# Performance work log

Measured on AMD Instinct MI355X. Metric: run time of the kernel, lower is better.

## Reference

```python
import jax, jax.numpy as jnp
import numpy as np

N_NODES = 50000
N_HEDGES = 20000
N_EDGES = 800000
D = 128
H = 4


def setup_inputs() -> dict:
    key = jax.random.key(0)
    ks = jax.random.split(key, 12)
    s = 1.0 / np.sqrt(D)
    return {
        "x_node": jax.random.normal(ks[0], (N_NODES, D), jnp.float32),
        "x_edge": jax.random.normal(ks[1], (N_HEDGES, D), jnp.float32),
        "src": jax.random.randint(ks[2], (N_EDGES,), 0, N_NODES, jnp.int32),
        "dst": jax.random.randint(ks[3], (N_EDGES,), 0, N_HEDGES, jnp.int32),
        "Wq": jax.random.normal(ks[4], (D, D), jnp.float32) * s,
        "bq": jnp.zeros((D,), jnp.float32),
        "Wk": jax.random.normal(ks[5], (D, D), jnp.float32) * s,
        "bk": jnp.zeros((D,), jnp.float32),
        "Wv": jax.random.normal(ks[6], (D, D), jnp.float32) * s,
        "bv": jnp.zeros((D,), jnp.float32),
        "Wo": jax.random.normal(ks[7], (D, D), jnp.float32) * s,
        "bo": jnp.zeros((D,), jnp.float32),
    }


def reference(x_node, x_edge, src, dst, Wq, bq, Wk, bk, Wv, bv, Wo, bo):
    N = x_node.shape[0]
    hd = Wq.shape[1] // H  # head_dim = 32
    Q = (x_node @ Wq + bq).reshape(N, H, hd)
    K = (x_edge @ Wk + bk).reshape(-1, H, hd)
    V = (x_edge @ Wv + bv).reshape(-1, H, hd)
    # per-edge gather: [E, H, hd]
    Qe = Q[src]
    Ke = K[dst]
    Ve = V[dst]
    # per-edge, per-head scores: [E, H]
    scores = jnp.einsum("ehd,ehd->eh", Qe, Ke) / jnp.sqrt(jnp.float32(hd))
    # segment softmax grouped by src node
    m = jax.ops.segment_max(scores, src, num_segments=N)  # [N, H]
    e = jnp.exp(scores - m[src])
    z = jax.ops.segment_sum(e, src, num_segments=N)  # [N, H]
    w = e / z[src]  # [E, H]
    # weighted scatter-add of V messages back to src nodes
    msg = w[:, :, None] * Ve  # [E, H, hd]
    out = jax.ops.segment_sum(msg, src, num_segments=N)  # [N, H, hd]
    out = out.reshape(N, -1)
    return out @ Wo + bo + x_node
```

## Files before the change

kernel.cpp:

```cpp
#include <hip/hip_runtime.h>

#define D 128
#define STRIDE 6144

typedef _Float16 f16;
typedef f16 f16x2 __attribute__((ext_vector_type(2)));
typedef f16 f16x8 __attribute__((ext_vector_type(8)));
typedef float f32x4 __attribute__((ext_vector_type(4)));

__device__ inline f16x2 u2h(unsigned u) { return __builtin_bit_cast(f16x2, u); }
__device__ inline unsigned h2u(f16x2 h) { return __builtin_bit_cast(unsigned, h); }

__device__ inline float dot2(unsigned a, unsigned b, float c) {
#if __has_builtin(__builtin_amdgcn_fdot2)
    return __builtin_amdgcn_fdot2(u2h(a), u2h(b), c, false);
#else
    f16x2 x = u2h(a), y = u2h(b);
    return c + (float)x.x * (float)y.x + (float)x.y * (float)y.y;
#endif
}

__global__ void wt_prep4(const float* __restrict__ W0, const float* __restrict__ W1,
                         const float* __restrict__ W2, const float* __restrict__ W3,
                         f16* __restrict__ Wt) {
    const float* W = (blockIdx.x == 0) ? W0 : (blockIdx.x == 1) ? W1 : (blockIdx.x == 2) ? W2 : W3;
    f16* o = Wt + (size_t)blockIdx.x * D * D;
    int t = threadIdx.x;
#pragma unroll
    for (int i = 0; i < 16; ++i) {
        int f = t + i * 256;
        int k = f >> 5, c4 = f & 31;
        float4 v = *(const float4*)(W + k * D + 4 * c4);
        float vv[4] = {v.x, v.y, v.z, v.w};
#pragma unroll
        for (int e = 0; e < 4; ++e) {
            int c = 4 * c4 + e;
            o[c * D + (((k >> 3) ^ (c & 15)) << 3) + (k & 7)] = (f16)vv[e];
        }
    }
}

__device__ inline void stage_w(const f16* __restrict__ Wt, f16* Wl, int t) {
#pragma unroll
    for (int i = 0; i < 8; ++i) ((uint4*)Wl)[t + i * 256] = ((const uint4*)Wt)[t + i * 256];
}

__device__ inline void load_a_f32(const float* __restrict__ x, int gr, int nrows, int g,
                                  f16x8 a[4]) {
#pragma unroll
    for (int kc = 0; kc < 4; ++kc) {
        float4 v0 = {0.f, 0.f, 0.f, 0.f}, v1 = {0.f, 0.f, 0.f, 0.f};
        if (gr < nrows) {
            const float* xr = x + (size_t)gr * D + (kc * 4 + g) * 8;
            v0 = *(const float4*)xr;
            v1 = *(const float4*)(xr + 4);
        }
        f16x8 af;
        af[0] = (f16)v0.x; af[1] = (f16)v0.y; af[2] = (f16)v0.z; af[3] = (f16)v0.w;
        af[4] = (f16)v1.x; af[5] = (f16)v1.y; af[6] = (f16)v1.z; af[7] = (f16)v1.w;
        a[kc] = af;
    }
}

__device__ inline void mfma_ra(const f16x8 a[4], const f16* Wl, f32x4 acc[8], int lane) {
    int lr = lane & 15, g = lane >> 4;
#pragma unroll
    for (int kc = 0; kc < 4; ++kc) {
        int slot = kc * 4 + g;
#pragma unroll
        for (int ct = 0; ct < 8; ++ct) {
            int col = ct * 16 + lr;
            f16x8 bf = *(const f16x8*)(Wl + col * D + ((slot ^ (col & 15)) << 3));
            acc[ct] = __builtin_amdgcn_mfma_f32_16x16x32_f16(a[kc], bf, acc[ct], 0, 0, 0);
        }
    }
}

__global__ __launch_bounds__(256) void fused_front(
    const float* __restrict__ x_node, const float* __restrict__ x_edge,
    const int* __restrict__ src, const int* __restrict__ dst,
    const f16* __restrict__ Wt,
    const float* __restrict__ bq, const float* __restrict__ bk, const float* __restrict__ bv,
    f16* __restrict__ Qh, f16* __restrict__ KVh,
    int* __restrict__ bucket_cnt, unsigned* __restrict__ temp,
    int N, int M, int E, int nsp, int nq, float qscale) {
    __shared__ __align__(16) f16 Wl[D * D];
    int t = threadIdx.x;
    int bid = blockIdx.x;

    if (bid < nsp) {
        int* hist = (int*)Wl;
        int* lex = hist + 256;
        int* gbase = lex + 256;
        int* lcur = gbase + 256;
        int* wsum = lcur + 256;
        int* sorted = wsum + 16;
        unsigned char* sbyte = (unsigned char*)(sorted + 4096);
        hist[t] = 0;
        lcur[t] = 0;
        __syncthreads();
        int base0 = bid * 4096;
        int lim = E - base0; if (lim > 4096) lim = 4096;
        for (int i = t; i < lim; i += 256) atomicAdd(&hist[src[base0 + i] >> 8], 1);
        __syncthreads();
        int v = hist[t];
        int inc = v;
#pragma unroll
        for (int m = 1; m < 64; m <<= 1) {
            int u = __shfl_up(inc, m);
            if ((t & 63) >= m) inc += u;
        }
        if ((t & 63) == 63) wsum[t >> 6] = inc;
        __syncthreads();
        int add = 0;
#pragma unroll
        for (int w = 0; w < 4; ++w)
            if (w < (t >> 6)) add += wsum[w];
        lex[t] = add + inc - v;
        if (v) gbase[t] = atomicAdd(&bucket_cnt[t], v);
        __syncthreads();
        for (int i = t; i < lim; i += 256) {
            int s = src[base0 + i];
            int bk2 = s >> 8;
            int lp = atomicAdd(&lcur[bk2], 1);
            int sp = lex[bk2] + lp;
            sorted[sp] = ((s & 255) << 24) | dst[base0 + i];
            sbyte[sp] = (unsigned char)bk2;
        }
        __syncthreads();
        for (int i = t; i < lim; i += 256) {
            int bk2 = sbyte[i];
            int gp = gbase[bk2] + (i - lex[bk2]);
            if (gp < STRIDE) temp[(size_t)bk2 * STRIDE + gp] = (unsigned)sorted[i];
        }
    } else if (bid < nsp + nq) {
        int r0 = (bid - nsp) * 64;
        stage_w(Wt, Wl, t);
        int lane = t & 63, w = t >> 6;
        int lr = lane & 15, g = lane >> 4;
        f16x8 a[4];
        load_a_f32(x_node, r0 + 16 * w + lr, N, g, a);
        f32x4 acc[8];
#pragma unroll
        for (int i = 0; i < 8; ++i) acc[i] = (f32x4){0.f, 0.f, 0.f, 0.f};
        __syncthreads();
        mfma_ra(a, Wl, acc, lane);
        __syncthreads();
#pragma unroll
        for (int ct = 0; ct < 8; ++ct) {
            int col = ct * 16 + lr;
            float bias = bq[col];
#pragma unroll
            for (int rg = 0; rg < 4; ++rg) {
                int row = 16 * w + 4 * g + rg;
                Wl[row * D + (((col >> 3) ^ (row & 15)) << 3) + (col & 7)] =
                    (f16)((acc[ct][rg] + bias) * qscale);
            }
        }
        __syncthreads();
#pragma unroll
        for (int i = 0; i < 4; ++i) {
            int f = t + i * 256;
            int r = f >> 4, c8 = f & 15;
            if (r0 + r < N) {
                uint4 v = *(const uint4*)(Wl + r * D + ((c8 ^ (r & 15)) << 3));
                *(uint4*)(Qh + (size_t)(r0 + r) * D + 8 * c8) = v;
            }
        }
    } else {
        int r0 = (bid - nsp - nq) * 64;
        stage_w(Wt + D * D, Wl, t);
        int lane = t & 63, w = t >> 6;
        int lr = lane & 15, g = lane >> 4;
        f16x8 a[4];
        load_a_f32(x_edge, r0 + 16 * w + lr, M, g, a);
        f32x4 accK[8], accV[8];
#pragma unroll
        for (int i = 0; i < 8; ++i) accK[i] = accV[i] = (f32x4){0.f, 0.f, 0.f, 0.f};
        __syncthreads();
        mfma_ra(a, Wl, accK, lane);
        __syncthreads();
        stage_w(Wt + 2 * D * D, Wl, t);
        __syncthreads();
        mfma_ra(a, Wl, accV, lane);
        __syncthreads();
#pragma unroll
        for (int ct = 0; ct < 8; ++ct) {
            int col = ct * 16 + lr;
            float bbk = bk[col], bbv = bv[col];
            int s = col >> 2, wk = col & 3;
#pragma unroll
            for (int rg = 0; rg < 4; ++rg) {
                int row = 16 * w + 4 * g + rg;
                f16* base = Wl + row * 256 + ((s ^ (row & 15)) << 3);
                base[wk] = (f16)(accK[ct][rg] + bbk);
                base[4 + wk] = (f16)(accV[ct][rg] + bbv);
            }
        }
        __syncthreads();
#pragma unroll
        for (int i = 0; i < 8; ++i) {
            int f = t + i * 256;
            int r = f >> 5, c8 = f & 31;
            if (r0 + r < M) {
                uint4 v = *(const uint4*)(Wl + r * 256 + ((c8 ^ (r & 15)) << 3));
                *(uint4*)(KVh + (size_t)(r0 + r) * 256 + 8 * c8) = v;
            }
        }
    }
}

__global__ __launch_bounds__(256) void bucket_scatter(const unsigned* __restrict__ temp,
                                                      const int* __restrict__ bucket_cnt,
                                                      int* __restrict__ off,
                                                      int* __restrict__ csr_dst,
                                                      int N, int E, int NBUK) {
    __shared__ int nh[256], cur[256], wsum[4], sc_ex[256], dh[256], dcur[256];
    __shared__ int sorted2[STRIDE];
    __shared__ int lds_dst[STRIDE];
    int b = blockIdx.x, t = threadIdx.x;
    {
        int bc = (t < NBUK) ? bucket_cnt[t] : 0;
        int inc = bc;
#pragma unroll
        for (int m = 1; m < 64; m <<= 1) {
            int u = __shfl_up(inc, m);
            if ((t & 63) >= m) inc += u;
        }
        if ((t & 63) == 63) wsum[t >> 6] = inc;
        __syncthreads();
        int add = 0;
#pragma unroll
        for (int w = 0; w < 4; ++w)
            if (w < (t >> 6)) add += wsum[w];
        sc_ex[t] = add + inc - bc;
        nh[t] = 0;
        dh[t] = 0;
    }
    __syncthreads();
    int bo = sc_ex[b];
    int cnt = bucket_cnt[b];
    if (cnt > STRIDE) cnt = STRIDE;
    const unsigned* tb = temp + (size_t)b * STRIDE;
    for (int i = t; i < cnt; i += 256) atomicAdd(&dh[(tb[i] & 0xFFFFFFu) >> 7], 1);
    __syncthreads();
    {
        int v = dh[t];
        int inc = v;
#pragma unroll
        for (int m = 1; m < 64; m <<= 1) {
            int u = __shfl_up(inc, m);
            if ((t & 63) >= m) inc += u;
        }
        if ((t & 63) == 63) wsum[t >> 6] = inc;
        __syncthreads();
        int add = 0;
#pragma unroll
        for (int w = 0; w < 4; ++w)
            if (w < (t >> 6)) add += wsum[w];
        dcur[t] = add + inc - v;
    }
    __syncthreads();
    for (int i = t; i < cnt; i += 256) {
        unsigned it = tb[i];
        int pos = atomicAdd(&dcur[(it & 0xFFFFFFu) >> 7], 1);
        sorted2[pos] = (int)it;
    }
    __syncthreads();
    for (int i = t; i < cnt; i += 256) atomicAdd(&nh[((unsigned)sorted2[i]) >> 24], 1);
    __syncthreads();
    {
        int v = nh[t];
        int inc = v;
#pragma unroll
        for (int m = 1; m < 64; m <<= 1) {
            int u = __shfl_up(inc, m);
            if ((t & 63) >= m) inc += u;
        }
        if ((t & 63) == 63) wsum[t >> 6] = inc;
        __syncthreads();
        int add = 0;
#pragma unroll
        for (int w = 0; w < 4; ++w)
            if (w < (t >> 6)) add += wsum[w];
        int ex = add + inc - v;
        cur[t] = ex;
        int node = (b << 8) + t;
        if (node < N) off[node] = bo + ex;
        if (b == 0 && t == 0) off[N] = E;
    }
    __syncthreads();
    for (int i = t; i < cnt; i += 256) {
        unsigned it = (unsigned)sorted2[i];
        int lpos = atomicAdd(&cur[it >> 24], 1);
        lds_dst[lpos] = (int)(it & 0xFFFFFFu);
    }
    __syncthreads();
    for (int i = t; i < cnt; i += 256) csr_dst[bo + i] = lds_dst[i];
}

__global__ __launch_bounds__(256) void node_attn4(const f16* __restrict__ Qh,
                                                  const f16* __restrict__ KVh,
                                                  const int* __restrict__ off,
                                                  const int* __restrict__ csr,
                                                  f16* __restrict__ aggh, int N) {
    int wid = (int)((blockIdx.x * (size_t)blockDim.x + threadIdx.x) >> 6);
    int lane = threadIdx.x & 63;
    if (wid >= N) return;
    int j = lane & 7, g = lane >> 3;
    const f16* qp = Qh + (size_t)wid * D + 16 * j;
    uint4 qA = *(const uint4*)qp;
    uint4 qB = *(const uint4*)(qp + 8);
    int beg = off[wid], end = off[wid + 1];
    float z = 0.f;
    f16x2 a0 = {0, 0}, a1 = {0, 0}, a2 = {0, 0}, a3 = {0, 0};
    f16x2 a4 = {0, 0}, a5 = {0, 0}, a6 = {0, 0}, a7 = {0, 0};
    if (beg < end) {
        int pe = beg + g;
        int d0 = csr[(pe < end) ? pe : end - 1];
        const f16* r = KVh + (size_t)d0 * 256 + 32 * j;
        uint4 A0 = *(const uint4*)r;
        uint4 A1 = *(const uint4*)(r + 8);
        uint4 A2 = *(const uint4*)(r + 16);
        uint4 A3 = *(const uint4*)(r + 24);
        for (int p = beg; p < end; p += 8) {
            int pn = p + 8 + g;
            int dn = csr[(pn < end) ? pn : end - 1];
            const f16* rn = KVh + (size_t)dn * 256 + 32 * j;
            uint4 B0 = *(const uint4*)rn;
            uint4 B1 = *(const uint4*)(rn + 8);
            uint4 B2 = *(const uint4*)(rn + 16);
            uint4 B3 = *(const uint4*)(rn + 24);
            bool valid = (p + g) < end;
            float s = dot2(A0.x, qA.x, 0.f);
            s = dot2(A0.y, qA.y, s);
            s = dot2(A1.x, qA.z, s);
            s = dot2(A1.y, qA.w, s);
            s = dot2(A2.x, qB.x, s);
            s = dot2(A2.y, qB.y, s);
            s = dot2(A3.x, qB.z, s);
            s = dot2(A3.y, qB.w, s);
            s += __shfl_xor(s, 1);
            float eh = valid ? __expf(s) : 0.f;
            z += eh;
            f16 e16 = (f16)eh;
            f16x2 e2 = {e16, e16};
            a0 += e2 * u2h(A0.z); a1 += e2 * u2h(A0.w);
            a2 += e2 * u2h(A1.z); a3 += e2 * u2h(A1.w);
            a4 += e2 * u2h(A2.z); a5 += e2 * u2h(A2.w);
            a6 += e2 * u2h(A3.z); a7 += e2 * u2h(A3.w);
            A0 = B0; A1 = B1; A2 = B2; A3 = B3;
        }
    }
#pragma unroll
    for (int m = 8; m < 64; m <<= 1) {
        z += __shfl_xor(z, m);
        a0 += u2h(__shfl_xor((int)h2u(a0), m));
        a1 += u2h(__shfl_xor((int)h2u(a1), m));
        a2 += u2h(__shfl_xor((int)h2u(a2), m));
        a3 += u2h(__shfl_xor((int)h2u(a3), m));
        a4 += u2h(__shfl_xor((int)h2u(a4), m));
        a5 += u2h(__shfl_xor((int)h2u(a5), m));
        a6 += u2h(__shfl_xor((int)h2u(a6), m));
        a7 += u2h(__shfl_xor((int)h2u(a7), m));
    }
    if (g == 0) {
        float inv = (end > beg) ? 1.f / z : 0.f;
        uint4 o0, o1;
        o0.x = h2u((f16x2){(f16)((float)a0.x * inv), (f16)((float)a0.y * inv)});
        o0.y = h2u((f16x2){(f16)((float)a1.x * inv), (f16)((float)a1.y * inv)});
        o0.z = h2u((f16x2){(f16)((float)a2.x * inv), (f16)((float)a2.y * inv)});
        o0.w = h2u((f16x2){(f16)((float)a3.x * inv), (f16)((float)a3.y * inv)});
        o1.x = h2u((f16x2){(f16)((float)a4.x * inv), (f16)((float)a4.y * inv)});
        o1.y = h2u((f16x2){(f16)((float)a5.x * inv), (f16)((float)a5.y * inv)});
        o1.z = h2u((f16x2){(f16)((float)a6.x * inv), (f16)((float)a6.y * inv)});
        o1.w = h2u((f16x2){(f16)((float)a7.x * inv), (f16)((float)a7.y * inv)});
        f16* op = aggh + (size_t)wid * D + 16 * j;
        *(uint4*)op = o0;
        *(uint4*)(op + 8) = o1;
    }
}

__global__ __launch_bounds__(256) void gemm_o(const f16* __restrict__ aggh,
                                              const f16* __restrict__ Wt,
                                              const float* __restrict__ b,
                                              const float* __restrict__ resid,
                                              float* __restrict__ y, int nrows) {
    __shared__ __align__(16) f16 Wl[D * D];
    int t = threadIdx.x;
    int r0 = blockIdx.x * 64;
    stage_w(Wt, Wl, t);
    int lane = t & 63, w = t >> 6;
    int lr = lane & 15, g = lane >> 4;
    int gr = r0 + 16 * w + lr;
    f16x8 a[4];
#pragma unroll
    for (int kc = 0; kc < 4; ++kc) {
        uint4 v = {0u, 0u, 0u, 0u};
        if (gr < nrows) v = *(const uint4*)(aggh + (size_t)gr * D + (kc * 4 + g) * 8);
        a[kc] = __builtin_bit_cast(f16x8, v);
    }
    f32x4 acc[8];
#pragma unroll
    for (int i = 0; i < 8; ++i) acc[i] = (f32x4){0.f, 0.f, 0.f, 0.f};
    __syncthreads();
    mfma_ra(a, Wl, acc, lane);
    __syncthreads();
    float* Tf = (float*)Wl;
#pragma unroll
    for (int ct = 0; ct < 8; ++ct) {
        int col = ct * 16 + lr;
        float bias = b[col];
        int s = col >> 2, wk = col & 3;
#pragma unroll
        for (int rg = 0; rg < 4; ++rg) {
            int row = 16 * w + 4 * g + rg;
            Tf[row * D + ((s ^ (row & 15)) << 2) + wk] = acc[ct][rg] + bias;
        }
    }
    __syncthreads();
#pragma unroll
    for (int i = 0; i < 8; ++i) {
        int f = t + i * 256;
        int r = f >> 5, c4 = f & 31;
        int gr2 = r0 + r;
        if (gr2 < nrows) {
            float4 v = *(const float4*)(Tf + r * D + ((c4 ^ (r & 15)) << 2));
            float4 rv = *(const float4*)(resid + (size_t)gr2 * D + 4 * c4);
            v.x += rv.x; v.y += rv.y; v.z += rv.z; v.w += rv.w;
            *(float4*)(y + (size_t)gr2 * D + 4 * c4) = v;
        }
    }
}

extern "C" void kernel_launch(void* const* d_in, const int* in_sizes, int n_in,
                              void* d_out, int out_size, void* d_ws, size_t ws_size,
                              hipStream_t stream) {
    const float* x_node = (const float*)d_in[0];
    const float* x_edge = (const float*)d_in[1];
    const int* src = (const int*)d_in[2];
    const int* dst = (const int*)d_in[3];
    const float* Wq = (const float*)d_in[4];
    const float* bq = (const float*)d_in[5];
    const float* Wk = (const float*)d_in[6];
    const float* bk = (const float*)d_in[7];
    const float* Wv = (const float*)d_in[8];
    const float* bv = (const float*)d_in[9];
    const float* Wo = (const float*)d_in[10];
    const float* bo = (const float*)d_in[11];

    int N = in_sizes[0] / D;
    int M = in_sizes[1] / D;
    int E = in_sizes[2];
    int NBUK = (N + 255) >> 8;

    char* p = (char*)d_ws;
    auto alloc = [&](size_t bytes) -> char* {
        char* r = p;
        p += (bytes + 15) & ~(size_t)15;
        return r;
    };
    f16* Wt = (f16*)alloc((size_t)4 * D * D * 2);
    f16* Qh = (f16*)alloc((size_t)N * D * 2);
    f16* KVh = (f16*)alloc((size_t)M * 256 * 2);
    f16* aggh = (f16*)alloc((size_t)N * D * 2);
    int* bucket_cnt = (int*)alloc(256 * 4);
    int* off = (int*)alloc((size_t)(N + 1) * 4);
    unsigned* temp = (unsigned*)alloc((size_t)NBUK * STRIDE * 4);
    int* csr_dst = (int*)alloc((size_t)E * 4);
    float* out = (float*)d_out;

    hipMemsetAsync(bucket_cnt, 0, 256 * 4, stream);

    wt_prep4<<<4, 256, 0, stream>>>(Wq, Wk, Wv, Wo, Wt);

    int nq = (N + 63) / 64;
    int nkv = (M + 63) / 64;
    int nsp = (E + 4095) / 4096;
    fused_front<<<nsp + nq + nkv, 256, 0, stream>>>(x_node, x_edge, src, dst, Wt,
                                                    bq, bk, bv, Qh, KVh,
                                                    bucket_cnt, temp,
                                                    N, M, E, nsp, nq, 0.17677669529663687f);

    bucket_scatter<<<NBUK, 256, 0, stream>>>(temp, bucket_cnt, off, csr_dst, N, E, NBUK);

    int ablk = (int)(((size_t)N * 64 + 255) / 256);
    node_attn4<<<ablk, 256, 0, stream>>>(Qh, KVh, off, csr_dst, aggh, N);

    gemm_o<<<(N + 63) / 64, 256, 0, stream>>>(aggh, Wt + 3 * D * D, bo, x_node, out, N);
}
```

Before: 114.0 us.

## Regroup kernels: fuse weight prep with bucket split, scatter with projections

Weight transpose/convert is merged into the same launch as the edge bucket-split pass, and the per-bucket CSR scatter is moved into the projection kernel as extra blocks. This drops one kernel launch and lets the scatter run concurrently with the Q/K/V GEMMs. The scatter now writes csr_dst directly from LDS-sorted positions instead of staging through a second LDS buffer. Scattered global writes may be less coalesced, and the scatter blocks share the 32KB LDS allocation with the GEMM blocks.

```diff
diff --git a/kernel.cpp b/kernel.cpp
--- a/kernel.cpp
+++ b/kernel.cpp
@@ -20,76 +20,31 @@
 #endif
 }
 
-__global__ void wt_prep4(const float* __restrict__ W0, const float* __restrict__ W1,
-                         const float* __restrict__ W2, const float* __restrict__ W3,
-                         f16* __restrict__ Wt) {
-    const float* W = (blockIdx.x == 0) ? W0 : (blockIdx.x == 1) ? W1 : (blockIdx.x == 2) ? W2 : W3;
-    f16* o = Wt + (size_t)blockIdx.x * D * D;
-    int t = threadIdx.x;
-#pragma unroll
-    for (int i = 0; i < 16; ++i) {
-        int f = t + i * 256;
-        int k = f >> 5, c4 = f & 31;
-        float4 v = *(const float4*)(W + k * D + 4 * c4);
-        float vv[4] = {v.x, v.y, v.z, v.w};
-#pragma unroll
-        for (int e = 0; e < 4; ++e) {
-            int c = 4 * c4 + e;
-            o[c * D + (((k >> 3) ^ (c & 15)) << 3) + (k & 7)] = (f16)vv[e];
-        }
-    }
-}
-
-__device__ inline void stage_w(const f16* __restrict__ Wt, f16* Wl, int t) {
-#pragma unroll
-    for (int i = 0; i < 8; ++i) ((uint4*)Wl)[t + i * 256] = ((const uint4*)Wt)[t + i * 256];
-}
-
-__device__ inline void load_a_f32(const float* __restrict__ x, int gr, int nrows, int g,
-                                  f16x8 a[4]) {
-#pragma unroll
-    for (int kc = 0; kc < 4; ++kc) {
-        float4 v0 = {0.f, 0.f, 0.f, 0.f}, v1 = {0.f, 0.f, 0.f, 0.f};
-        if (gr < nrows) {
-            const float* xr = x + (size_t)gr * D + (kc * 4 + g) * 8;
-            v0 = *(const float4*)xr;
-            v1 = *(const float4*)(xr + 4);
-        }
-        f16x8 af;
-        af[0] = (f16)v0.x; af[1] = (f16)v0.y; af[2] = (f16)v0.z; af[3] = (f16)v0.w;
-        af[4] = (f16)v1.x; af[5] = (f16)v1.y; af[6] = (f16)v1.z; af[7] = (f16)v1.w;
-        a[kc] = af;
-    }
-}
-
-__device__ inline void mfma_ra(const f16x8 a[4], const f16* Wl, f32x4 acc[8], int lane) {
-    int lr = lane & 15, g = lane >> 4;
-#pragma unroll
-    for (int kc = 0; kc < 4; ++kc) {
-        int slot = kc * 4 + g;
-#pragma unroll
-        for (int ct = 0; ct < 8; ++ct) {
-            int col = ct * 16 + lr;
-            f16x8 bf = *(const f16x8*)(Wl + col * D + ((slot ^ (col & 15)) << 3));
-            acc[ct] = __builtin_amdgcn_mfma_f32_16x16x32_f16(a[kc], bf, acc[ct], 0, 0, 0);
-        }
-    }
-}
-
-__global__ __launch_bounds__(256) void fused_front(
-    const float* __restrict__ x_node, const float* __restrict__ x_edge,
+__global__ __launch_bounds__(256) void prep_split(
+    const float* __restrict__ Wq, const float* __restrict__ Wk,
+    const float* __restrict__ Wv, const float* __restrict__ Wo,
     const int* __restrict__ src, const int* __restrict__ dst,
-    const f16* __restrict__ Wt,
-    const float* __restrict__ bq, const float* __restrict__ bk, const float* __restrict__ bv,
-    f16* __restrict__ Qh, f16* __restrict__ KVh,
-    int* __restrict__ bucket_cnt, unsigned* __restrict__ temp,
-    int N, int M, int E, int nsp, int nq, float qscale) {
-    __shared__ __align__(16) f16 Wl[D * D];
+    f16* __restrict__ Wt, int* __restrict__ bucket_cnt, unsigned* __restrict__ temp, int E) {
+    __shared__ __align__(16) int smem[6400 + 1024];
     int t = threadIdx.x;
     int bid = blockIdx.x;
-
-    if (bid < nsp) {
-        int* hist = (int*)Wl;
+    if (bid < 4) {
+        const float* W = (bid == 0) ? Wq : (bid == 1) ? Wk : (bid == 2) ? Wv : Wo;
+        f16* o = Wt + (size_t)bid * D * D;
+#pragma unroll
+        for (int i = 0; i < 16; ++i) {
+            int f = t + i * 256;
+            int k = f >> 5, c4 = f & 31;
+            float4 v = *(const float4*)(W + k * D + 4 * c4);
+            float vv[4] = {v.x, v.y, v.z, v.w};
+#pragma unroll
+            for (int e = 0; e < 4; ++e) {
+                int c = 4 * c4 + e;
+                o[c * D + (((k >> 3) ^ (c & 15)) << 3) + (k & 7)] = (f16)vv[e];
+            }
+        }
+    } else {
+        int* hist = smem;
         int* lex = hist + 256;
         int* gbase = lex + 256;
         int* lcur = gbase + 256;
@@ -99,7 +54,7 @@
         hist[t] = 0;
         lcur[t] = 0;
         __syncthreads();
-        int base0 = bid * 4096;
+        int base0 = (bid - 4) * 4096;
         int lim = E - base0; if (lim > 4096) lim = 4096;
         for (int i = t; i < lim; i += 256) atomicAdd(&hist[src[base0 + i] >> 8], 1);
         __syncthreads();
@@ -133,8 +88,144 @@
             int gp = gbase[bk2] + (i - lex[bk2]);
             if (gp < STRIDE) temp[(size_t)bk2 * STRIDE + gp] = (unsigned)sorted[i];
         }
-    } else if (bid < nsp + nq) {
-        int r0 = (bid - nsp) * 64;
+    }
+}
+
+__device__ inline void stage_w(const f16* __restrict__ Wt, f16* Wl, int t) {
+#pragma unroll
+    for (int i = 0; i < 8; ++i) ((uint4*)Wl)[t + i * 256] = ((const uint4*)Wt)[t + i * 256];
+}
+
+__device__ inline void load_a_f32(const float* __restrict__ x, int gr, int nrows, int g,
+                                  f16x8 a[4]) {
+#pragma unroll
+    for (int kc = 0; kc < 4; ++kc) {
+        float4 v0 = {0.f, 0.f, 0.f, 0.f}, v1 = {0.f, 0.f, 0.f, 0.f};
+        if (gr < nrows) {
+            const float* xr = x + (size_t)gr * D + (kc * 4 + g) * 8;
+            v0 = *(const float4*)xr;
+            v1 = *(const float4*)(xr + 4);
+        }
+        f16x8 af;
+        af[0] = (f16)v0.x; af[1] = (f16)v0.y; af[2] = (f16)v0.z; af[3] = (f16)v0.w;
+        af[4] = (f16)v1.x; af[5] = (f16)v1.y; af[6] = (f16)v1.z; af[7] = (f16)v1.w;
+        a[kc] = af;
+    }
+}
+
+__device__ inline void mfma_ra(const f16x8 a[4], const f16* Wl, f32x4 acc[8], int lane) {
+    int lr = lane & 15, g = lane >> 4;
+#pragma unroll
+    for (int kc = 0; kc < 4; ++kc) {
+        int slot = kc * 4 + g;
+#pragma unroll
+        for (int ct = 0; ct < 8; ++ct) {
+            int col = ct * 16 + lr;
+            f16x8 bf = *(const f16x8*)(Wl + col * D + ((slot ^ (col & 15)) << 3));
+            acc[ct] = __builtin_amdgcn_mfma_f32_16x16x32_f16(a[kc], bf, acc[ct], 0, 0, 0);
+        }
+    }
+}
+
+__global__ __launch_bounds__(256) void fused_front(
+    const float* __restrict__ x_node, const float* __restrict__ x_edge,
+    const f16* __restrict__ Wt,
+    const float* __restrict__ bq, const float* __restrict__ bk, const float* __restrict__ bv,
+    f16* __restrict__ Qh, f16* __restrict__ KVh,
+    const unsigned* __restrict__ temp, const int* __restrict__ bucket_cnt,
+    int* __restrict__ off, int* __restrict__ csr_dst,
+    int N, int M, int E, int nsc, int nq, int NBUK, float qscale) {
+    __shared__ __align__(16) f16 Wl[D * D];
+    int t = threadIdx.x;
+    int bid = blockIdx.x;
+
+    if (bid < nsc) {
+        int* nh = (int*)Wl;
+        int* cur = nh + 256;
+        int* wsum = cur + 256;
+        int* sc_ex = wsum + 16;
+        int* dh = sc_ex + 256;
+        int* dcur = dh + 256;
+        int* sorted2 = dcur + 256;
+        int b = bid;
+        {
+            int bc = (t < NBUK) ? bucket_cnt[t] : 0;
+            int inc = bc;
+#pragma unroll
+            for (int m = 1; m < 64; m <<= 1) {
+                int u = __shfl_up(inc, m);
+                if ((t & 63) >= m) inc += u;
+            }
+            if ((t & 63) == 63) wsum[t >> 6] = inc;
+            __syncthreads();
+            int add = 0;
+#pragma unroll
+            for (int w = 0; w < 4; ++w)
+                if (w < (t >> 6)) add += wsum[w];
+            sc_ex[t] = add + inc - bc;
+            nh[t] = 0;
+            dh[t] = 0;
+        }
+        __syncthreads();
+        int bo = sc_ex[b];
+        int cnt = bucket_cnt[b];
+        if (cnt > STRIDE) cnt = STRIDE;
+        const unsigned* tb = temp + (size_t)b * STRIDE;
+        for (int i = t; i < cnt; i += 256) atomicAdd(&dh[(tb[i] & 0xFFFFFFu) >> 7], 1);
+        __syncthreads();
+        {
+            int v = dh[t];
+            int inc = v;
+#pragma unroll
+            for (int m = 1; m < 64; m <<= 1) {
+                int u = __shfl_up(inc, m);
+                if ((t & 63) >= m) inc += u;
+            }
+            if ((t & 63) == 63) wsum[t >> 6] = inc;
+            __syncthreads();
+            int add = 0;
+#pragma unroll
+            for (int w = 0; w < 4; ++w)
+                if (w < (t >> 6)) add += wsum[w];
+            dcur[t] = add + inc - v;
+        }
+        __syncthreads();
+        for (int i = t; i < cnt; i += 256) {
+            unsigned it = tb[i];
+            int pos = atomicAdd(&dcur[(it & 0xFFFFFFu) >> 7], 1);
+            sorted2[pos] = (int)it;
+        }
+        __syncthreads();
+        for (int i = t; i < cnt; i += 256) atomicAdd(&nh[((unsigned)sorted2[i]) >> 24], 1);
+        __syncthreads();
+        {
+            int v = nh[t];
+            int inc = v;
+#pragma unroll
+            for (int m = 1; m < 64; m <<= 1) {
+                int u = __shfl_up(inc, m);
+                if ((t & 63) >= m) inc += u;
+            }
+            if ((t & 63) == 63) wsum[t >> 6] = inc;
+            __syncthreads();
+            int add = 0;
+#pragma unroll
+            for (int w = 0; w < 4; ++w)
+                if (w < (t >> 6)) add += wsum[w];
+            int ex = add + inc - v;
+            cur[t] = ex;
+            int node = (b << 8) + t;
+            if (node < N) off[node] = bo + ex;
+            if (b == 0 && t == 0) off[N] = E;
+        }
+        __syncthreads();
+        for (int i = t; i < cnt; i += 256) {
+            unsigned it = (unsigned)sorted2[i];
+            int lpos = atomicAdd(&cur[it >> 24], 1);
+            csr_dst[bo + lpos] = (int)(it & 0xFFFFFFu);
+        }
+    } else if (bid < nsc + nq) {
+        int r0 = (bid - nsc) * 64;
         stage_w(Wt, Wl, t);
         int lane = t & 63, w = t >> 6;
         int lr = lane & 15, g = lane >> 4;
@@ -168,7 +259,7 @@
             }
         }
     } else {
-        int r0 = (bid - nsp - nq) * 64;
+        int r0 = (bid - nsc - nq) * 64;
         stage_w(Wt + D * D, Wl, t);
         int lane = t & 63, w = t >> 6;
         int lr = lane & 15, g = lane >> 4;
@@ -208,95 +299,6 @@
             }
         }
     }
-}
-
-__global__ __launch_bounds__(256) void bucket_scatter(const unsigned* __restrict__ temp,
-                                                      const int* __restrict__ bucket_cnt,
-                                                      int* __restrict__ off,
-                                                      int* __restrict__ csr_dst,
-                                                      int N, int E, int NBUK) {
-    __shared__ int nh[256], cur[256], wsum[4], sc_ex[256], dh[256], dcur[256];
-    __shared__ int sorted2[STRIDE];
-    __shared__ int lds_dst[STRIDE];
-    int b = blockIdx.x, t = threadIdx.x;
-    {
-        int bc = (t < NBUK) ? bucket_cnt[t] : 0;
-        int inc = bc;
-#pragma unroll
-        for (int m = 1; m < 64; m <<= 1) {
-            int u = __shfl_up(inc, m);
-            if ((t & 63) >= m) inc += u;
-        }
-        if ((t & 63) == 63) wsum[t >> 6] = inc;
-        __syncthreads();
-        int add = 0;
-#pragma unroll
-        for (int w = 0; w < 4; ++w)
-            if (w < (t >> 6)) add += wsum[w];
-        sc_ex[t] = add + inc - bc;
-        nh[t] = 0;
-        dh[t] = 0;
-    }
-    __syncthreads();
-    int bo = sc_ex[b];
-    int cnt = bucket_cnt[b];
-    if (cnt > STRIDE) cnt = STRIDE;
-    const unsigned* tb = temp + (size_t)b * STRIDE;
-    for (int i = t; i < cnt; i += 256) atomicAdd(&dh[(tb[i] & 0xFFFFFFu) >> 7], 1);
-    __syncthreads();
-    {
-        int v = dh[t];
-        int inc = v;
-#pragma unroll
-        for (int m = 1; m < 64; m <<= 1) {
-            int u = __shfl_up(inc, m);
-            if ((t & 63) >= m) inc += u;
-        }
-        if ((t & 63) == 63) wsum[t >> 6] = inc;
-        __syncthreads();
-        int add = 0;
-#pragma unroll
-        for (int w = 0; w < 4; ++w)
-            if (w < (t >> 6)) add += wsum[w];
-        dcur[t] = add + inc - v;
-    }
-    __syncthreads();
-    for (int i = t; i < cnt; i += 256) {
-        unsigned it = tb[i];
-        int pos = atomicAdd(&dcur[(it & 0xFFFFFFu) >> 7], 1);
-        sorted2[pos] = (int)it;
-    }
-    __syncthreads();
-    for (int i = t; i < cnt; i += 256) atomicAdd(&nh[((unsigned)sorted2[i]) >> 24], 1);
-    __syncthreads();
-    {
-        int v = nh[t];
-        int inc = v;
-#pragma unroll
-        for (int m = 1; m < 64; m <<= 1) {
-            int u = __shfl_up(inc, m);
-            if ((t & 63) >= m) inc += u;
-        }
-        if ((t & 63) == 63) wsum[t >> 6] = inc;
-        __syncthreads();
-        int add = 0;
-#pragma unroll
-        for (int w = 0; w < 4; ++w)
-            if (w < (t >> 6)) add += wsum[w];
-        int ex = add + inc - v;
-        cur[t] = ex;
-        int node = (b << 8) + t;
-        if (node < N) off[node] = bo + ex;
-        if (b == 0 && t == 0) off[N] = E;
-    }
-    __syncthreads();
-    for (int i = t; i < cnt; i += 256) {
-        unsigned it = (unsigned)sorted2[i];
-        int lpos = atomicAdd(&cur[it >> 24], 1);
-        lds_dst[lpos] = (int)(it & 0xFFFFFFu);
-    }
-    __syncthreads();
-    for (int i = t; i < cnt; i += 256) csr_dst[bo + i] = lds_dst[i];
 }
 
 __global__ __launch_bounds__(256) void node_attn4(const f16* __restrict__ Qh,
@@ -472,17 +474,18 @@
 
     hipMemsetAsync(bucket_cnt, 0, 256 * 4, stream);
 
-    wt_prep4<<<4, 256, 0, stream>>>(Wq, Wk, Wv, Wo, Wt);
-
+    int nsp = (E + 4095) / 4096;
     int nq = (N + 63) / 64;
     int nkv = (M + 63) / 64;
-    int nsp = (E + 4095) / 4096;
-    fused_front<<<nsp + nq + nkv, 256, 0, stream>>>(x_node, x_edge, src, dst, Wt,
-                                                    bq, bk, bv, Qh, KVh,
-                                                    bucket_cnt, temp,
-                                                    N, M, E, nsp, nq, 0.17677669529663687f);
-
-    bucket_scatter<<<NBUK, 256, 0, stream>>>(temp, bucket_cnt, off, csr_dst, N, E, NBUK);
+
+    prep_split<<<4 + nsp, 256, 0, stream>>>(Wq, Wk, Wv, Wo, src, dst,
+                                            Wt, bucket_cnt, temp, E);
+
+    fused_front<<<NBUK + nq + nkv, 256, 0, stream>>>(x_node, x_edge, Wt,
+                                                     bq, bk, bv, Qh, KVh,
+                                                     temp, bucket_cnt, off, csr_dst,
+                                                     N, M, E, NBUK, nq, NBUK,
+                                                     0.17677669529663687f);
 
     int ablk = (int)(((size_t)N * 64 + 255) / 256);
     node_attn4<<<ablk, 256, 0, stream>>>(Qh, KVh, off, csr_dst, aggh, N);
```

Result: faster. 107.6 us (-5.7%).
